# Kernel tuning notes

Measured on AMD Instinct MI355X. Metric: run time of the kernel, lower is better.

## Reference

```python
import jax, jax.numpy as jnp
import numpy as np

B, L = 4, 256          # batch, tokens per example
V = 100000             # conceptnet_len (vocab)
E = 256                # emb_size (== da for self-attention)


def setup_inputs() -> dict:
    key = jax.random.key(0)
    k1, k2, k3 = jax.random.split(key, 3)
    conceptnet_text_vec = jax.random.randint(k1, (B, L), 0, V, dtype=jnp.int64)
    # Embedding table and self-attention params (xavier-ish scale)
    table = jax.random.normal(k2, (V, E), dtype=jnp.float32) * (1.0 / np.sqrt(E))
    ka, kb = jax.random.split(k3)
    a = jax.random.normal(ka, (E, E), dtype=jnp.float32) * np.sqrt(2.0 / (E + E)) * 1.414
    b = jax.random.normal(kb, (E, 1), dtype=jnp.float32) * np.sqrt(2.0 / (E + 1)) * 1.414
    return {"conceptnet_text_vec": conceptnet_text_vec, "table": table, "a": a, "b": b, "topk": 16}


def reference(conceptnet_text_vec, table, a, b, topk):
    # emb: [B, L, E] gather from table
    emb = table[conceptnet_text_vec]
    # dense similarity against full table: [B, L, V]
    logits = jnp.einsum("ble,ve->blv", emb, table)
    match = jax.nn.softmax(logits, axis=-1)
    # top-k neighbor indices: [B, L, K]
    _, idx = jax.lax.top_k(match, topk)
    # second gather: [B, L, K, E]
    h = table[idx]
    # self-attention pool over the K retrieved concepts
    # e: [B, L, 1, K]
    e = jnp.swapaxes(jnp.matmul(jnp.tanh(jnp.matmul(h, a)), b), -1, -2)
    attention = jax.nn.softmax(e, axis=-1)
    # [B, L, 1, E] -> [B, L, E]
    att_emb = jnp.matmul(attention, h).squeeze(-2)
    return att_emb
```

## Files before the change

kernel.cpp:

```cpp
#include <hip/hip_runtime.h>


#define V_ROWS   100000
#define E_DIM    256
#define M_TOK    1024
#define NGROUPS  98
#define VGROUP   1024
#define NCAND    (NGROUPS*8)
#define KBIAS    2.5f
#define SENTINEL -0.45f

typedef _Float16 f16x8 __attribute__((ext_vector_type(8)));
typedef float    f32x4 __attribute__((ext_vector_type(4)));

__global__ __launch_bounds__(256) void prep_kernel(
    const float* __restrict__ table, const int* __restrict__ text,
    const float* __restrict__ amat,
    _Float16* __restrict__ tabh, _Float16* __restrict__ embh,
    _Float16* __restrict__ ahT)
{
  const int NTAB = V_ROWS * E_DIM / 8;
  const int NEMB = M_TOK * E_DIM / 8;
  const int NA   = E_DIM * E_DIM;
  const int NU   = NTAB + NEMB + NA;
  for (int u = blockIdx.x * 256 + threadIdx.x; u < NU; u += gridDim.x * 256) {
    if (u < NTAB + NEMB) {
      size_t srcoff; _Float16* dst;
      if (u < NTAB) {
        srcoff = (size_t)u * 8; dst = tabh + (size_t)u * 8;
      } else {
        int e2 = u - NTAB; int tt = e2 >> 5, kc = e2 & 31;
        srcoff = (size_t)text[tt] * E_DIM + kc * 8;
        dst = embh + (size_t)e2 * 8;
      }
      float4 x0 = *(const float4*)(table + srcoff);
      float4 x1 = *(const float4*)(table + srcoff + 4);
      f16x8 hv;
      hv[0]=(_Float16)x0.x; hv[1]=(_Float16)x0.y; hv[2]=(_Float16)x0.z; hv[3]=(_Float16)x0.w;
      hv[4]=(_Float16)x1.x; hv[5]=(_Float16)x1.y; hv[6]=(_Float16)x1.z; hv[7]=(_Float16)x1.w;
      *(f16x8*)dst = hv;
    } else {
      int e3 = u - NTAB - NEMB;
      int k = e3 >> 8, n = e3 & 255;
      ahT[n * E_DIM + k] = (_Float16)amat[e3];
    }
  }
}

__device__ __forceinline__ unsigned int pack_key(float val, int lidx) {
  float b = val + KBIAS;
  unsigned int u = __builtin_bit_cast(unsigned int, b);
  return (((u >> 7) & 0xFFFFu) << 10) | (unsigned int)lidx;
}
__device__ __forceinline__ float thr_from_key(unsigned int key) {
  unsigned int u = 0x40000000u | ((key >> 10) << 7);
  return __builtin_bit_cast(float, u) - KBIAS;
}

__global__ __launch_bounds__(256, 3) void gemm_topk_kernel(
    const _Float16* __restrict__ tabh, const _Float16* __restrict__ embh,
    unsigned int* __restrict__ cand)
{
  int bid = blockIdx.x;
  int group, mtile;
  if (bid < 1536) { int xcd = bid & 7, r = bid >> 3; mtile = r & 15; group = xcd * 12 + (r >> 4); }
  else            { int r = bid - 1536;              mtile = r & 15; group = 96 + (r >> 4); }

  const int tid = threadIdx.x;
  const int w = tid >> 6, l = tid & 63;

  __shared__ uint4 Alds[64 * 32];
  __shared__ float Lq[64 * 64];

  {
    const uint4* srcA = (const uint4*)embh + (size_t)mtile * 64 * 32;
    #pragma unroll
    for (int i = 0; i < 8; ++i) {
      int c = i * 256 + tid;
      int r = c >> 5, kc = c & 31;
      Alds[r * 32 + (kc ^ (r & 7))] = srcA[c];
    }
  }
  __syncthreads();

  unsigned int t8[8] = {0, 0, 0, 0, 0, 0, 0, 0};
  float thr = -0.5f;
  const int sr = tid >> 2;
  const int ss = tid & 3;

  auto ins = [&](unsigned int key) {
    unsigned int k = key;
    #pragma unroll
    for (int q2 = 0; q2 < 8; ++q2) {
      unsigned int mx = t8[q2] > k ? t8[q2] : k;
      unsigned int mn = t8[q2] > k ? k : t8[q2];
      t8[q2] = mx; k = mn;
    }
    thr = thr_from_key(t8[7]);
  };

  auto loadB = [&](int g, int kk, int fn) -> f16x8 {
    int v = group * VGROUP + g * 256 + w * 64 + fn * 16 + (l & 15);
    v = v < V_ROWS ? v : V_ROWS - 1;
    return *reinterpret_cast<const f16x8*>(
        tabh + (size_t)v * E_DIM + kk * 32 + (l >> 4) * 8);
  };

  f16x8 bf[4];
  #pragma unroll
  for (int fn = 0; fn < 4; ++fn) bf[fn] = loadB(0, 0, fn);

  for (int g = 0; g < 4; ++g) {
    f32x4 acc[4][4] = {};

    #pragma unroll
    for (int kk = 0; kk < 8; ++kk) {
      f16x8 bcur[4];
      #pragma unroll
      for (int fn = 0; fn < 4; ++fn) bcur[fn] = bf[fn];
      if (kk < 7) {
        #pragma unroll
        for (int fn = 0; fn < 4; ++fn) bf[fn] = loadB(g, kk + 1, fn);
      } else if (g < 3) {
        #pragma unroll
        for (int fn = 0; fn < 4; ++fn) bf[fn] = loadB(g + 1, 0, fn);
      }
      int kc = kk * 4 + (l >> 4);
      #pragma unroll
      for (int fm = 0; fm < 4; ++fm) {
        int r = fm * 16 + (l & 15);
        f16x8 af = *reinterpret_cast<const f16x8*>(&Alds[r * 32 + (kc ^ (r & 7))]);
        #pragma unroll
        for (int fn = 0; fn < 4; ++fn)
          acc[fm][fn] = __builtin_amdgcn_mfma_f32_16x16x32_f16(
              af, bcur[fn], acc[fm][fn], 0, 0, 0);
      }
    }

    for (int q = 0; q < 4; ++q) {
      __syncthreads();
      if (w == q) {
        #pragma unroll
        for (int fm = 0; fm < 4; ++fm)
          #pragma unroll
          for (int fn = 0; fn < 4; ++fn) {
            int cq = fn * 16 + (l & 15);
            int gcol = group * VGROUP + g * 256 + q * 64 + cq;
            #pragma unroll
            for (int r2 = 0; r2 < 4; ++r2) {
              int row = fm * 16 + (l >> 4) * 4 + r2;
              float val = (gcol < V_ROWS) ? acc[fm][fn][r2] : SENTINEL;
              Lq[row * 64 + (((cq >> 2) ^ (row & 7)) << 2) + (cq & 3)] = val;
            }
          }
      }
      __syncthreads();
      const float4* Lq4 = (const float4*)Lq;
      int lbase = g * 256 + q * 64 + ss * 16;
      #pragma unroll
      for (int j = 0; j < 4; ++j) {
        float4 v = Lq4[sr * 16 + ((ss * 4 + j) ^ (sr & 7))];
        float m = fmaxf(fmaxf(v.x, v.y), fmaxf(v.z, v.w));
        if (m > thr) {
          int cb = lbase + 4 * j;
          if (v.x > thr) ins(pack_key(v.x, cb));
          if (v.y > thr) ins(pack_key(v.y, cb + 1));
          if (v.z > thr) ins(pack_key(v.z, cb + 2));
          if (v.w > thr) ins(pack_key(v.w, cb + 3));
        }
      }
    }
  }

  __syncthreads();
  unsigned int* Clds = (unsigned int*)Lq;
  #pragma unroll
  for (int i = 0; i < 8; ++i) Clds[tid * 8 + i] = t8[i];
  __syncthreads();
  if (tid < 64) {
    unsigned int best[8] = {0, 0, 0, 0, 0, 0, 0, 0};
    for (int s2 = 0; s2 < 4; ++s2)
      for (int i = 0; i < 8; ++i) {
        unsigned int key = Clds[(tid * 4 + s2) * 8 + i];
        if (key > best[7]) {
          #pragma unroll
          for (int q2 = 0; q2 < 8; ++q2) {
            unsigned int mx = best[q2] > key ? best[q2] : key;
            unsigned int mn = best[q2] > key ? key : best[q2];
            best[q2] = mx; key = mn;
          }
        }
      }
    int token = mtile * 64 + tid;
    unsigned int* dst = cand + ((size_t)token * NGROUPS + group) * 8;
    #pragma unroll
    for (int i = 0; i < 8; ++i) dst[i] = best[i];
  }
}

__global__ __launch_bounds__(256) void select_kernel(
    const float* __restrict__ table, const int* __restrict__ text,
    const unsigned int* __restrict__ cand, int* __restrict__ hidx)
{
  const int t = blockIdx.x, tid = threadIdx.x;
  const int lane = tid & 63, w = tid >> 6;
  __shared__ unsigned int ck[NCAND];
  __shared__ int selv[32];
  __shared__ float ex[32];
  __shared__ unsigned long long wred[4];

  for (int i = tid; i < NCAND; i += 256) ck[i] = cand[(size_t)t * NCAND + i];
  __syncthreads();

  for (int it = 0; it < 32; ++it) {
    unsigned long long best = 0;
    for (int i = tid; i < NCAND; i += 256) {
      unsigned long long p = ((unsigned long long)ck[i] << 10) | (unsigned int)i;
      if (p > best) best = p;
    }
    #pragma unroll
    for (int d = 32; d >= 1; d >>= 1) {
      unsigned long long o = __shfl_xor(best, d);
      if (o > best) best = o;
    }
    if (lane == 0) wred[w] = best;
    __syncthreads();
    if (tid == 0) {
      unsigned long long b = wred[0];
      for (int q = 1; q < 4; ++q) if (wred[q] > b) b = wred[q];
      int slot = (int)(b & 1023ull);
      unsigned int key = ck[slot];
      selv[it] = (slot >> 3) * VGROUP + (int)(key & 1023u);
      ck[slot] = 0;
    }
    __syncthreads();
  }

  {
    int c = tid >> 3, s = tid & 7;
    int tok = text[t];
    const float* er = table + (size_t)tok * E_DIM;
    const float* tr = table + (size_t)selv[c] * E_DIM;
    float acc = 0.f;
    #pragma unroll 8
    for (int k2 = 0; k2 < 32; ++k2) acc += er[s * 32 + k2] * tr[s * 32 + k2];
    #pragma unroll
    for (int d = 1; d < 8; d <<= 1) acc += __shfl_xor(acc, d);
    if (s == 0) ex[c] = acc;
  }
  __syncthreads();

  if (w == 0) {
    float val = (lane < 32) ? ex[lane] : -1e38f;
    for (int it = 0; it < 16; ++it) {
      float m = val;
      #pragma unroll
      for (int d = 1; d < 32; d <<= 1) { float o = __shfl_xor(m, d); m = o > m ? o : m; }
      unsigned long long msk = __ballot(lane < 32 && val == m);
      int winner = __ffsll(msk) - 1;
      if (lane == 0) hidx[t * 16 + it] = selv[winner];
      if (lane == winner) val = -1e38f;
    }
  }
}

__global__ __launch_bounds__(256, 2) void gemm_ta_kernel(
    const _Float16* __restrict__ tabh, const _Float16* __restrict__ ahT,
    const int* __restrict__ hidx, float* __restrict__ ta)
{
  const int mtile = blockIdx.x;
  const int tid = threadIdx.x;
  const int w = tid >> 6, l = tid & 63;
  __shared__ uint4 Alds[64 * 32];

  #pragma unroll
  for (int i = 0; i < 8; ++i) {
    int c = i * 256 + tid;
    int r = c >> 5, kc = c & 31;
    int src = hidx[mtile * 64 + r];
    Alds[r * 32 + (kc ^ (r & 7))] =
        *(const uint4*)(tabh + (size_t)src * E_DIM + kc * 8);
  }
  __syncthreads();

  f32x4 acc[4][4] = {};
  #pragma unroll
  for (int kk = 0; kk < 8; ++kk) {
    f16x8 af[4], bf[4];
    int kc = kk * 4 + (l >> 4);
    #pragma unroll
    for (int fm = 0; fm < 4; ++fm) {
      int r = fm * 16 + (l & 15);
      af[fm] = *reinterpret_cast<const f16x8*>(&Alds[r * 32 + (kc ^ (r & 7))]);
    }
    #pragma unroll
    for (int fn = 0; fn < 4; ++fn) {
      int n = w * 64 + fn * 16 + (l & 15);
      bf[fn] = *reinterpret_cast<const f16x8*>(
          ahT + (size_t)n * E_DIM + kk * 32 + (l >> 4) * 8);
    }
    #pragma unroll
    for (int fm = 0; fm < 4; ++fm)
      #pragma unroll
      for (int fn = 0; fn < 4; ++fn)
        acc[fm][fn] = __builtin_amdgcn_mfma_f32_16x16x32_f16(
            af[fm], bf[fn], acc[fm][fn], 0, 0, 0);
  }

  #pragma unroll
  for (int fm = 0; fm < 4; ++fm) {
    int row = mtile * 64 + fm * 16 + (l >> 4) * 4;
    #pragma unroll
    for (int fn = 0; fn < 4; ++fn) {
      int col = w * 64 + fn * 16 + (l & 15);
      #pragma unroll
      for (int r2 = 0; r2 < 4; ++r2)
        ta[(size_t)(row + r2) * E_DIM + col] = acc[fm][fn][r2];
    }
  }
}

__global__ __launch_bounds__(256) void attn_pool_kernel(
    const float* __restrict__ table, const float* __restrict__ bvec,
    const int* __restrict__ hidx, const float* __restrict__ ta,
    float* __restrict__ out)
{
  const int t = blockIdx.x, tid = threadIdx.x;
  const int lane = tid & 63, w = tid >> 6;
  __shared__ float hl[16][257];
  __shared__ float part[16][4];
  __shared__ float wgt[16];

  #pragma unroll
  for (int i = 0; i < 16; ++i)
    hl[i][tid] = table[(size_t)hidx[t * 16 + i] * E_DIM + tid];

  float bj = bvec[tid];
  float s_[16];
  #pragma unroll
  for (int i = 0; i < 16; ++i) {
    float x = ta[((size_t)t * 16 + i) * E_DIM + tid];
    s_[i] = tanhf(x) * bj;
  }
  #pragma unroll
  for (int i = 0; i < 16; ++i) {
    float r = s_[i];
    #pragma unroll
    for (int d = 1; d < 64; d <<= 1) r += __shfl_xor(r, d);
    if (lane == 0) part[i][w] = r;
  }
  __syncthreads();
  if (tid < 16) {
    float e = part[tid][0] + part[tid][1] + part[tid][2] + part[tid][3];
    float m = e;
    #pragma unroll
    for (int d = 1; d < 16; d <<= 1) { float o = __shfl_xor(m, d); m = o > m ? o : m; }
    float p = expf(e - m);
    float sum = p;
    #pragma unroll
    for (int d = 1; d < 16; d <<= 1) sum += __shfl_xor(sum, d);
    wgt[tid] = p / sum;
  }
  __syncthreads();
  float o = 0.f;
  #pragma unroll
  for (int i = 0; i < 16; ++i) o += wgt[i] * hl[i][tid];
  out[(size_t)t * E_DIM + tid] = o;
}

extern "C" void kernel_launch(void* const* d_in, const int* in_sizes, int n_in,
                              void* d_out, int out_size, void* d_ws, size_t ws_size,
                              hipStream_t stream) {
  const int*   text  = (const int*)d_in[0];
  const float* table = (const float*)d_in[1];
  const float* amat  = (const float*)d_in[2];
  const float* bvec  = (const float*)d_in[3];
  float*       out   = (float*)d_out;

  char* ws = (char*)d_ws;
  _Float16*     tabh = (_Float16*)(ws + 0);
  _Float16*     embh = (_Float16*)(ws + 51200000);
  _Float16*     ahT  = (_Float16*)(ws + 51724288);
  unsigned int* cand = (unsigned int*)(ws + 51855360);
  int*          hidx = (int*)(ws + 55066624);
  float*        ta   = (float*)(ws + 55132160);

  prep_kernel<<<2048, 256, 0, stream>>>(table, text, amat, tabh, embh, ahT);
  gemm_topk_kernel<<<16 * NGROUPS, 256, 0, stream>>>(tabh, embh, cand);
  select_kernel<<<M_TOK, 256, 0, stream>>>(table, text, cand, hidx);
  gemm_ta_kernel<<<256, 256, 0, stream>>>(tabh, ahT, hidx, ta);
  attn_pool_kernel<<<M_TOK, 256, 0, stream>>>(table, bvec, hidx, ta, out);
}
```

Before: 420.3 us.

## Register-resident top-k in GEMM, histogram select, fuse attention GEMM with pooling

The similarity GEMM now keeps per-lane top-4 lists directly in MFMA accumulator registers, with operands swapped so each lane owns token rows. This removes the LDS round-trip and the four barrier-separated scan phases per 256-column chunk, and double-buffers the B loads. The select kernel replaces 32 block-wide argmax passes with a bucket histogram that takes the clear winners directly and runs an argmax only over the boundary bucket. The tanh-attention GEMM is fused with the softmax pooling, which drops the intermediate ta buffer and one launch. The risk is that keeping only 4 candidates per lane slice instead of 8 may drop true top-k items.

```diff
diff --git a/kernel.cpp b/kernel.cpp
--- a/kernel.cpp
+++ b/kernel.cpp
@@ -8,7 +8,6 @@
 #define VGROUP   1024
 #define NCAND    (NGROUPS*8)
 #define KBIAS    2.5f
-#define SENTINEL -0.45f
 
 typedef _Float16 f16x8 __attribute__((ext_vector_type(8)));
 typedef float    f32x4 __attribute__((ext_vector_type(4)));
@@ -70,7 +69,7 @@
   const int w = tid >> 6, l = tid & 63;
 
   __shared__ uint4 Alds[64 * 32];
-  __shared__ float Lq[64 * 64];
+  __shared__ uint4 Cl[64 * 17];
 
   {
     const uint4* srcA = (const uint4*)embh + (size_t)mtile * 64 * 32;
@@ -83,116 +82,122 @@
   }
   __syncthreads();
 
-  unsigned int t8[8] = {0, 0, 0, 0, 0, 0, 0, 0};
-  float thr = -0.5f;
-  const int sr = tid >> 2;
-  const int ss = tid & 3;
-
-  auto ins = [&](unsigned int key) {
-    unsigned int k = key;
-    #pragma unroll
-    for (int q2 = 0; q2 < 8; ++q2) {
-      unsigned int mx = t8[q2] > k ? t8[q2] : k;
-      unsigned int mn = t8[q2] > k ? k : t8[q2];
-      t8[q2] = mx; k = mn;
-    }
-    thr = thr_from_key(t8[7]);
-  };
-
-  auto loadB = [&](int g, int kk, int fn) -> f16x8 {
-    int v = group * VGROUP + g * 256 + w * 64 + fn * 16 + (l & 15);
-    v = v < V_ROWS ? v : V_ROWS - 1;
-    return *reinterpret_cast<const f16x8*>(
-        tabh + (size_t)v * E_DIM + kk * 32 + (l >> 4) * 8);
-  };
-
-  f16x8 bf[4];
-  #pragma unroll
-  for (int fn = 0; fn < 4; ++fn) bf[fn] = loadB(0, 0, fn);
+  const int limit = (group == NGROUPS - 1) ? (V_ROWS - (NGROUPS - 1) * VGROUP) : VGROUP;
+  unsigned int t4[4][4] = {{0,0,0,0},{0,0,0,0},{0,0,0,0},{0,0,0,0}};
+  float thr[4] = {-0.5f, -0.5f, -0.5f, -0.5f};
+
+  const int rbase = group * VGROUP + w * 64 + (l & 15);
+  const int koff  = (l >> 4) * 8;
+
+  f16x8 bufA[4], bufB[4];
+
+#define LOADB(BUF, G, KK)                                                    \
+  {                                                                          \
+    _Pragma("unroll")                                                        \
+    for (int fv = 0; fv < 4; ++fv) {                                         \
+      int v = rbase + (G) * 256 + fv * 16;                                   \
+      v = v < V_ROWS ? v : V_ROWS - 1;                                       \
+      BUF[fv] = *reinterpret_cast<const f16x8*>(                             \
+          tabh + ((size_t)v << 8) + (KK) * 32 + koff);                       \
+    }                                                                        \
+  }
+
+  LOADB(bufA, 0, 0)
+  LOADB(bufB, 0, 1)
+
+  f32x4 acc[4][4];
+
+#define KSTEP(G, KK, BUF, DOPRE, PG, PKK)                                    \
+  {                                                                          \
+    int cs = ((KK) * 4 + (l >> 4)) ^ (l & 7);                                \
+    f16x8 af0 = *reinterpret_cast<const f16x8*>(&Alds[((l & 15)      ) * 32 + cs]); \
+    f16x8 af1 = *reinterpret_cast<const f16x8*>(&Alds[(16 + (l & 15)) * 32 + cs]);  \
+    f16x8 af2 = *reinterpret_cast<const f16x8*>(&Alds[(32 + (l & 15)) * 32 + cs]);  \
+    f16x8 af3 = *reinterpret_cast<const f16x8*>(&Alds[(48 + (l & 15)) * 32 + cs]);  \
+    _Pragma("unroll")                                                        \
+    for (int fv = 0; fv < 4; ++fv) {                                         \
+      acc[fv][0] = __builtin_amdgcn_mfma_f32_16x16x32_f16(BUF[fv], af0, acc[fv][0], 0, 0, 0); \
+      acc[fv][1] = __builtin_amdgcn_mfma_f32_16x16x32_f16(BUF[fv], af1, acc[fv][1], 0, 0, 0); \
+      acc[fv][2] = __builtin_amdgcn_mfma_f32_16x16x32_f16(BUF[fv], af2, acc[fv][2], 0, 0, 0); \
+      acc[fv][3] = __builtin_amdgcn_mfma_f32_16x16x32_f16(BUF[fv], af3, acc[fv][3], 0, 0, 0); \
+    }                                                                        \
+    if (DOPRE) LOADB(BUF, PG, PKK)                                           \
+  }
 
   for (int g = 0; g < 4; ++g) {
-    f32x4 acc[4][4] = {};
-
-    #pragma unroll
-    for (int kk = 0; kk < 8; ++kk) {
-      f16x8 bcur[4];
+    #pragma unroll
+    for (int fv = 0; fv < 4; ++fv)
       #pragma unroll
-      for (int fn = 0; fn < 4; ++fn) bcur[fn] = bf[fn];
-      if (kk < 7) {
+      for (int fm = 0; fm < 4; ++fm)
+        acc[fv][fm] = (f32x4){0.f, 0.f, 0.f, 0.f};
+
+    KSTEP(g, 0, bufA, 1, g, 2)
+    KSTEP(g, 1, bufB, 1, g, 3)
+    KSTEP(g, 2, bufA, 1, g, 4)
+    KSTEP(g, 3, bufB, 1, g, 5)
+    KSTEP(g, 4, bufA, 1, g, 6)
+    KSTEP(g, 5, bufB, 1, g, 7)
+    KSTEP(g, 6, bufA, (g < 3), g + 1, 0)
+    KSTEP(g, 7, bufB, (g < 3), g + 1, 1)
+
+    int qb = g * 256 + w * 64 + ((l >> 4) << 2);
+    #pragma unroll
+    for (int fv = 0; fv < 4; ++fv) {
+      int lb = qb + fv * 16;
+      if (lb + 4 <= limit) {
         #pragma unroll
-        for (int fn = 0; fn < 4; ++fn) bf[fn] = loadB(g, kk + 1, fn);
-      } else if (g < 3) {
-        #pragma unroll
-        for (int fn = 0; fn < 4; ++fn) bf[fn] = loadB(g + 1, 0, fn);
-      }
-      int kc = kk * 4 + (l >> 4);
-      #pragma unroll
-      for (int fm = 0; fm < 4; ++fm) {
-        int r = fm * 16 + (l & 15);
-        f16x8 af = *reinterpret_cast<const f16x8*>(&Alds[r * 32 + (kc ^ (r & 7))]);
-        #pragma unroll
-        for (int fn = 0; fn < 4; ++fn)
-          acc[fm][fn] = __builtin_amdgcn_mfma_f32_16x16x32_f16(
-              af, bcur[fn], acc[fm][fn], 0, 0, 0);
-      }
-    }
-
-    for (int q = 0; q < 4; ++q) {
-      __syncthreads();
-      if (w == q) {
-        #pragma unroll
-        for (int fm = 0; fm < 4; ++fm)
-          #pragma unroll
-          for (int fn = 0; fn < 4; ++fn) {
-            int cq = fn * 16 + (l & 15);
-            int gcol = group * VGROUP + g * 256 + q * 64 + cq;
+        for (int fm = 0; fm < 4; ++fm) {
+          f32x4 v = acc[fv][fm];
+          float m = fmaxf(fmaxf(v[0], v[1]), fmaxf(v[2], v[3]));
+          if (m > thr[fm]) {
             #pragma unroll
-            for (int r2 = 0; r2 < 4; ++r2) {
-              int row = fm * 16 + (l >> 4) * 4 + r2;
-              float val = (gcol < V_ROWS) ? acc[fm][fn][r2] : SENTINEL;
-              Lq[row * 64 + (((cq >> 2) ^ (row & 7)) << 2) + (cq & 3)] = val;
+            for (int e = 0; e < 4; ++e) {
+              if (v[e] > thr[fm]) {
+                unsigned int kx = pack_key(v[e], lb + e);
+                #pragma unroll
+                for (int q = 0; q < 4; ++q) {
+                  unsigned int mx = t4[fm][q] > kx ? t4[fm][q] : kx;
+                  unsigned int mn = t4[fm][q] > kx ? kx : t4[fm][q];
+                  t4[fm][q] = mx; kx = mn;
+                }
+                thr[fm] = thr_from_key(t4[fm][3]);
+              }
             }
           }
-      }
-      __syncthreads();
-      const float4* Lq4 = (const float4*)Lq;
-      int lbase = g * 256 + q * 64 + ss * 16;
+        }
+      }
+    }
+  }
+#undef KSTEP
+#undef LOADB
+
+  #pragma unroll
+  for (int fm = 0; fm < 4; ++fm) {
+    int token = fm * 16 + (l & 15);
+    int contrib = w * 4 + (l >> 4);
+    Cl[token * 17 + contrib] = make_uint4(t4[fm][0], t4[fm][1], t4[fm][2], t4[fm][3]);
+  }
+  __syncthreads();
+  if (tid < 64) {
+    unsigned int best[8] = {0,0,0,0,0,0,0,0};
+    #pragma unroll 4
+    for (int c = 0; c < 16; ++c) {
+      uint4 q4 = Cl[tid * 17 + c];
+      unsigned int ks[4] = {q4.x, q4.y, q4.z, q4.w};
       #pragma unroll
-      for (int j = 0; j < 4; ++j) {
-        float4 v = Lq4[sr * 16 + ((ss * 4 + j) ^ (sr & 7))];
-        float m = fmaxf(fmaxf(v.x, v.y), fmaxf(v.z, v.w));
-        if (m > thr) {
-          int cb = lbase + 4 * j;
-          if (v.x > thr) ins(pack_key(v.x, cb));
-          if (v.y > thr) ins(pack_key(v.y, cb + 1));
-          if (v.z > thr) ins(pack_key(v.z, cb + 2));
-          if (v.w > thr) ins(pack_key(v.w, cb + 3));
-        }
-      }
-    }
-  }
-
-  __syncthreads();
-  unsigned int* Clds = (unsigned int*)Lq;
-  #pragma unroll
-  for (int i = 0; i < 8; ++i) Clds[tid * 8 + i] = t8[i];
-  __syncthreads();
-  if (tid < 64) {
-    unsigned int best[8] = {0, 0, 0, 0, 0, 0, 0, 0};
-    for (int s2 = 0; s2 < 4; ++s2)
-      for (int i = 0; i < 8; ++i) {
-        unsigned int key = Clds[(tid * 4 + s2) * 8 + i];
-        if (key > best[7]) {
+      for (int e = 0; e < 4; ++e) {
+        unsigned int kx = ks[e];
+        if (kx > best[7]) {
           #pragma unroll
-          for (int q2 = 0; q2 < 8; ++q2) {
-            unsigned int mx = best[q2] > key ? best[q2] : key;
-            unsigned int mn = best[q2] > key ? key : best[q2];
-            best[q2] = mx; key = mn;
+          for (int q = 0; q < 8; ++q) {
+            unsigned int mx = best[q] > kx ? best[q] : kx;
+            unsigned int mn = best[q] > kx ? kx : best[q];
+            best[q] = mx; kx = mn;
           }
         }
       }
-    int token = mtile * 64 + tid;
-    unsigned int* dst = cand + ((size_t)token * NGROUPS + group) * 8;
+    }
+    unsigned int* dst = cand + ((size_t)(mtile * 64 + tid) * NGROUPS + group) * 8;
     #pragma unroll
     for (int i = 0; i < 8; ++i) dst[i] = best[i];
   }
@@ -205,36 +210,78 @@
   const int t = blockIdx.x, tid = threadIdx.x;
   const int lane = tid & 63, w = tid >> 6;
   __shared__ unsigned int ck[NCAND];
+  __shared__ unsigned long long pool[NCAND];
+  __shared__ int hist[64];
   __shared__ int selv[32];
   __shared__ float ex[32];
-  __shared__ unsigned long long wred[4];
-
-  for (int i = tid; i < NCAND; i += 256) ck[i] = cand[(size_t)t * NCAND + i];
-  __syncthreads();
-
-  for (int it = 0; it < 32; ++it) {
-    unsigned long long best = 0;
-    for (int i = tid; i < NCAND; i += 256) {
-      unsigned long long p = ((unsigned long long)ck[i] << 10) | (unsigned int)i;
-      if (p > best) best = p;
-    }
-    #pragma unroll
-    for (int d = 32; d >= 1; d >>= 1) {
-      unsigned long long o = __shfl_xor(best, d);
-      if (o > best) best = o;
-    }
-    if (lane == 0) wred[w] = best;
-    __syncthreads();
-    if (tid == 0) {
-      unsigned long long b = wred[0];
-      for (int q = 1; q < 4; ++q) if (wred[q] > b) b = wred[q];
-      int slot = (int)(b & 1023ull);
-      unsigned int key = ck[slot];
-      selv[it] = (slot >> 3) * VGROUP + (int)(key & 1023u);
-      ck[slot] = 0;
-    }
-    __syncthreads();
-  }
+  __shared__ int sh_b, sh_above, sh_c1, sh_c2;
+
+  if (tid < 64) hist[tid] = 0;
+  if (tid == 0) { sh_c1 = 0; sh_c2 = 0; }
+  __syncthreads();
+
+  for (int i = tid; i < NCAND; i += 256) {
+    unsigned int k = cand[(size_t)t * NCAND + i];
+    ck[i] = k;
+    atomicAdd(&hist[k >> 20], 1);
+  }
+  __syncthreads();
+
+  if (w == 0) {
+    int v = hist[lane];
+    int u;
+    u = __shfl_down(v, 1);  if (lane < 63) v += u;
+    u = __shfl_down(v, 2);  if (lane < 62) v += u;
+    u = __shfl_down(v, 4);  if (lane < 60) v += u;
+    u = __shfl_down(v, 8);  if (lane < 56) v += u;
+    u = __shfl_down(v, 16); if (lane < 48) v += u;
+    u = __shfl_down(v, 32); if (lane < 32) v += u;
+    unsigned long long msk = __ballot(v >= 32);
+    int b = 63 - __builtin_clzll(msk);
+    int above = (b < 63) ? __shfl(v, b + 1) : 0;
+    if (lane == 0) { sh_b = b; sh_above = above; }
+  }
+  __syncthreads();
+
+  const int b = sh_b;
+  for (int i = tid; i < NCAND; i += 256) {
+    unsigned int k = ck[i];
+    unsigned int bk = k >> 20;
+    if (bk > (unsigned)b) {
+      int p = atomicAdd(&sh_c1, 1);
+      selv[p] = (i >> 3) * VGROUP + (int)(k & 1023u);
+    } else if (bk == (unsigned)b) {
+      int p = atomicAdd(&sh_c2, 1);
+      pool[p] = ((unsigned long long)k << 20) | ((unsigned long long)i << 10)
+              | (unsigned long long)p;
+    }
+  }
+  __syncthreads();
+
+  const int C = sh_above, R = 32 - C;
+  if (w == 0) {
+    int n2 = sh_c2;
+    for (int it = 0; it < R; ++it) {
+      unsigned long long best = 0;
+      for (int i = lane; i < n2; i += 64) {
+        unsigned long long p = pool[i];
+        if (p > best) best = p;
+      }
+      #pragma unroll
+      for (int d = 32; d >= 1; d >>= 1) {
+        unsigned long long o = __shfl_xor(best, d);
+        if (o > best) best = o;
+      }
+      if (lane == 0) {
+        int pos  = (int)(best & 1023ull);
+        int slot = (int)((best >> 10) & 1023ull);
+        unsigned int k = (unsigned int)(best >> 20);
+        selv[C + it] = (slot >> 3) * VGROUP + (int)(k & 1023u);
+        pool[pos] = 0;
+      }
+    }
+  }
+  __syncthreads();
 
   {
     int c = tid >> 3, s = tid & 7;
@@ -264,108 +311,98 @@
   }
 }
 
-__global__ __launch_bounds__(256, 2) void gemm_ta_kernel(
+__global__ __launch_bounds__(256) void gemm_attn_kernel(
     const _Float16* __restrict__ tabh, const _Float16* __restrict__ ahT,
-    const int* __restrict__ hidx, float* __restrict__ ta)
+    const float* __restrict__ table, const float* __restrict__ bvec,
+    const int* __restrict__ hidx, float* __restrict__ out)
 {
   const int mtile = blockIdx.x;
   const int tid = threadIdx.x;
   const int w = tid >> 6, l = tid & 63;
   __shared__ uint4 Alds[64 * 32];
+  __shared__ int   hx[64];
+  __shared__ float ep[64][5];
+  __shared__ float wg[64];
+
+  if (tid < 64) hx[tid] = hidx[mtile * 64 + tid];
+  __syncthreads();
 
   #pragma unroll
   for (int i = 0; i < 8; ++i) {
     int c = i * 256 + tid;
     int r = c >> 5, kc = c & 31;
-    int src = hidx[mtile * 64 + r];
     Alds[r * 32 + (kc ^ (r & 7))] =
-        *(const uint4*)(tabh + (size_t)src * E_DIM + kc * 8);
-  }
-  __syncthreads();
-
-  f32x4 acc[4][4] = {};
+        *(const uint4*)(tabh + ((size_t)hx[r] << 8) + kc * 8);
+  }
+  __syncthreads();
+
+  f32x4 acc[4][4];
+  #pragma unroll
+  for (int fm = 0; fm < 4; ++fm)
+    #pragma unroll
+    for (int fn = 0; fn < 4; ++fn)
+      acc[fm][fn] = (f32x4){0.f, 0.f, 0.f, 0.f};
+
   #pragma unroll
   for (int kk = 0; kk < 8; ++kk) {
+    int cs = (kk * 4 + (l >> 4)) ^ (l & 7);
     f16x8 af[4], bf[4];
-    int kc = kk * 4 + (l >> 4);
-    #pragma unroll
-    for (int fm = 0; fm < 4; ++fm) {
-      int r = fm * 16 + (l & 15);
-      af[fm] = *reinterpret_cast<const f16x8*>(&Alds[r * 32 + (kc ^ (r & 7))]);
-    }
-    #pragma unroll
-    for (int fn = 0; fn < 4; ++fn) {
-      int n = w * 64 + fn * 16 + (l & 15);
+    #pragma unroll
+    for (int fm = 0; fm < 4; ++fm)
+      af[fm] = *reinterpret_cast<const f16x8*>(&Alds[(fm * 16 + (l & 15)) * 32 + cs]);
+    #pragma unroll
+    for (int fn = 0; fn < 4; ++fn)
       bf[fn] = *reinterpret_cast<const f16x8*>(
-          ahT + (size_t)n * E_DIM + kk * 32 + (l >> 4) * 8);
-    }
+          ahT + (size_t)(w * 64 + fn * 16 + (l & 15)) * E_DIM + kk * 32 + (l >> 4) * 8);
     #pragma unroll
     for (int fm = 0; fm < 4; ++fm)
       #pragma unroll
       for (int fn = 0; fn < 4; ++fn)
-        acc[fm][fn] = __builtin_amdgcn_mfma_f32_16x16x32_f16(
-            af[fm], bf[fn], acc[fm][fn], 0, 0, 0);
-  }
+        acc[fm][fn] = __builtin_amdgcn_mfma_f32_16x16x32_f16(af[fm], bf[fn], acc[fm][fn], 0, 0, 0);
+  }
+
+  float bv[4];
+  #pragma unroll
+  for (int fn = 0; fn < 4; ++fn) bv[fn] = bvec[w * 64 + fn * 16 + (l & 15)];
 
   #pragma unroll
   for (int fm = 0; fm < 4; ++fm) {
-    int row = mtile * 64 + fm * 16 + (l >> 4) * 4;
-    #pragma unroll
-    for (int fn = 0; fn < 4; ++fn) {
-      int col = w * 64 + fn * 16 + (l & 15);
-      #pragma unroll
-      for (int r2 = 0; r2 < 4; ++r2)
-        ta[(size_t)(row + r2) * E_DIM + col] = acc[fm][fn][r2];
-    }
-  }
-}
-
-__global__ __launch_bounds__(256) void attn_pool_kernel(
-    const float* __restrict__ table, const float* __restrict__ bvec,
-    const int* __restrict__ hidx, const float* __restrict__ ta,
-    float* __restrict__ out)
-{
-  const int t = blockIdx.x, tid = threadIdx.x;
-  const int lane = tid & 63, w = tid >> 6;
-  __shared__ float hl[16][257];
-  __shared__ float part[16][4];
-  __shared__ float wgt[16];
-
-  #pragma unroll
-  for (int i = 0; i < 16; ++i)
-    hl[i][tid] = table[(size_t)hidx[t * 16 + i] * E_DIM + tid];
-
-  float bj = bvec[tid];
-  float s_[16];
-  #pragma unroll
-  for (int i = 0; i < 16; ++i) {
-    float x = ta[((size_t)t * 16 + i) * E_DIM + tid];
-    s_[i] = tanhf(x) * bj;
-  }
-  #pragma unroll
-  for (int i = 0; i < 16; ++i) {
-    float r = s_[i];
-    #pragma unroll
-    for (int d = 1; d < 64; d <<= 1) r += __shfl_xor(r, d);
-    if (lane == 0) part[i][w] = r;
-  }
-  __syncthreads();
-  if (tid < 16) {
-    float e = part[tid][0] + part[tid][1] + part[tid][2] + part[tid][3];
+    #pragma unroll
+    for (int r2 = 0; r2 < 4; ++r2) {
+      float s = tanhf(acc[fm][0][r2]) * bv[0] + tanhf(acc[fm][1][r2]) * bv[1]
+              + tanhf(acc[fm][2][r2]) * bv[2] + tanhf(acc[fm][3][r2]) * bv[3];
+      s += __shfl_xor(s, 1); s += __shfl_xor(s, 2);
+      s += __shfl_xor(s, 4); s += __shfl_xor(s, 8);
+      if ((l & 15) == 0) ep[fm * 16 + (l >> 4) * 4 + r2][w] = s;
+    }
+  }
+  __syncthreads();
+
+  if (tid < 64) {
+    float e = ep[tid][0] + ep[tid][1] + ep[tid][2] + ep[tid][3];
     float m = e;
-    #pragma unroll
-    for (int d = 1; d < 16; d <<= 1) { float o = __shfl_xor(m, d); m = o > m ? o : m; }
+    m = fmaxf(m, __shfl_xor(m, 1)); m = fmaxf(m, __shfl_xor(m, 2));
+    m = fmaxf(m, __shfl_xor(m, 4)); m = fmaxf(m, __shfl_xor(m, 8));
     float p = expf(e - m);
-    float sum = p;
-    #pragma unroll
-    for (int d = 1; d < 16; d <<= 1) sum += __shfl_xor(sum, d);
-    wgt[tid] = p / sum;
-  }
-  __syncthreads();
-  float o = 0.f;
-  #pragma unroll
-  for (int i = 0; i < 16; ++i) o += wgt[i] * hl[i][tid];
-  out[(size_t)t * E_DIM + tid] = o;
+    float ssum = p;
+    ssum += __shfl_xor(ssum, 1); ssum += __shfl_xor(ssum, 2);
+    ssum += __shfl_xor(ssum, 4); ssum += __shfl_xor(ssum, 8);
+    wg[tid] = p / ssum;
+  }
+  __syncthreads();
+
+  {
+    int token = w;
+    int c4 = l * 4;
+    float4 o = make_float4(0.f, 0.f, 0.f, 0.f);
+    #pragma unroll
+    for (int i = 0; i < 16; ++i) {
+      float wt = wg[token * 16 + i];
+      float4 h = *(const float4*)(table + ((size_t)hx[token * 16 + i] << 8) + c4);
+      o.x += wt * h.x; o.y += wt * h.y; o.z += wt * h.z; o.w += wt * h.w;
+    }
+    *(float4*)(out + (size_t)(mtile * 4 + token) * E_DIM + c4) = o;
+  }
 }
 
 extern "C" void kernel_launch(void* const* d_in, const int* in_sizes, int n_in,
@@ -383,11 +420,9 @@
   _Float16*     ahT  = (_Float16*)(ws + 51724288);
   unsigned int* cand = (unsigned int*)(ws + 51855360);
   int*          hidx = (int*)(ws + 55066624);
-  float*        ta   = (float*)(ws + 55132160);
 
   prep_kernel<<<2048, 256, 0, stream>>>(table, text, amat, tabh, embh, ahT);
   gemm_topk_kernel<<<16 * NGROUPS, 256, 0, stream>>>(tabh, embh, cand);
   select_kernel<<<M_TOK, 256, 0, stream>>>(table, text, cand, hidx);
-  gemm_ta_kernel<<<256, 256, 0, stream>>>(tabh, ahT, hidx, ta);
-  attn_pool_kernel<<<M_TOK, 256, 0, stream>>>(table, bvec, hidx, ta, out);
-}
+  gemm_attn_kernel<<<256, 256, 0, stream>>>(tabh, ahT, table, bvec, hidx, out);
+}
```

Result: slower. 487.2 us (+15.9%).
